# Performance work log

Measured on AMD Instinct MI355X. Metric: run time of the kernel, lower is better.

The kernel has to match this reference:

```python
import jax, jax.numpy as jnp
import numpy as np

B = 64            # graphs
N0 = 1024         # nodes per graph at level 0
DEG = 16          # avg degree
D = 128
NS = [1024, 820, 656, 525, 420, 336]  # ceil(0.8*n) cascade


def gcn(x, src, dst, valid, W, b, num_nodes):
    # x: [N,D]; src/dst: [E] int; valid: [E] float mask; W: [D,D]; b: [D]
    x = x @ W.T + b
    deg = jax.ops.segment_sum(valid, src, num_segments=num_nodes) + 1.0  # +1 self loop
    dis = jax.lax.rsqrt(deg)
    norm = dis[src] * dis[dst] * valid
    agg = jax.ops.segment_sum(norm[:, None] * x[src], dst, num_segments=num_nodes)
    return agg + (dis * dis)[:, None] * x  # self-loop term


def topk_pool(x, src, dst, valid, w, n, k):
    # PyG TopKPooling: score = tanh((x.w)/||w||); keep top ceil(ratio*n) per graph
    s = jnp.tanh((x @ w) / jnp.linalg.norm(w))
    _, idx = jax.lax.top_k(s.reshape(B, n), k)                    # [B,k] local ids
    perm = (idx + (jnp.arange(B) * n)[:, None]).reshape(-1)       # global ids
    xn = x[perm] * s[perm][:, None]
    new_id = jnp.full((B * n,), -1, jnp.int32).at[perm].set(jnp.arange(B * k, dtype=jnp.int32))
    ns_, nd_ = new_id[src], new_id[dst]
    v = valid * ((ns_ >= 0) & (nd_ >= 0)).astype(jnp.float32)
    return xn, jnp.maximum(ns_, 0), jnp.maximum(nd_, 0), v


def setup_inputs() -> dict:
    key = jax.random.key(0)
    ks = jax.random.split(key, 32)
    x = jax.random.normal(ks[0], (B * N0, D), jnp.float32)
    eg = N0 * DEG  # edges per graph
    local = jax.random.randint(ks[1], (2, B, eg), 0, N0, jnp.int32)
    edge_index = (local + (jnp.arange(B, dtype=jnp.int32) * N0)[None, :, None]).reshape(2, -1)
    batch = jnp.repeat(jnp.arange(B, dtype=jnp.int32), N0)
    sc = 1.0 / np.sqrt(D)
    inp = {"x": x, "edge_index": edge_index, "batch": batch}
    for i in range(1, 6):
        inp[f"c{i}w"] = jax.random.normal(ks[2 * i], (D, D), jnp.float32) * sc
        inp[f"c{i}b"] = jnp.zeros((D,), jnp.float32)
        inp[f"p{i}w"] = jax.random.normal(ks[2 * i + 1], (D,), jnp.float32) * sc
    inp["l1w"] = jax.random.normal(ks[20], (128, 256), jnp.float32) / np.sqrt(256)
    inp["l1b"] = jnp.zeros((128,), jnp.float32)
    inp["l2w"] = jax.random.normal(ks[21], (64, 128), jnp.float32) * sc
    inp["l2b"] = jnp.zeros((64,), jnp.float32)
    inp["l3w"] = jax.random.normal(ks[22], (2, 64), jnp.float32) / np.sqrt(64)
    inp["l3b"] = jnp.zeros((2,), jnp.float32)
    return inp


def reference(x, edge_index, batch,
              c1w, c1b, p1w, c2w, c2b, p2w, c3w, c3b, p3w,
              c4w, c4b, p4w, c5w, c5b, p5w,
              l1w, l1b, l2w, l2b, l3w, l3b):
    src, dst = edge_index[0], edge_index[1]
    valid = jnp.ones(src.shape, jnp.float32)
    layers = [(c1w, c1b, p1w), (c2w, c2b, p2w), (c3w, c3b, p3w),
              (c4w, c4b, p4w), (c5w, c5b, p5w)]
    reads = []
    for i, (cw, cb, pw) in enumerate(layers):
        n, k = NS[i], NS[i + 1]
        x = jax.nn.relu(gcn(x, src, dst, valid, cw, cb, B * n))
        x, src, dst, valid = topk_pool(x, src, dst, valid, pw, n, k)
        xk = x.reshape(B, k, D)
        reads.append(jnp.concatenate([xk.max(axis=1), xk.mean(axis=1)], axis=1))
    h = reads[0] + reads[1] + reads[2] + reads[3] + reads[4]   # [B,256]
    h = jax.nn.relu(h @ l1w.T + l1b)
    # dropout is identity in eval mode
    h = jax.nn.relu(h @ l2w.T + l2b)
    return jax.nn.log_softmax(h @ l3w.T + l3b, axis=-1)       # [B,2]
```

## Files before the change

### kernel.cpp

```cpp
#include <hip/hip_runtime.h>
#include <hip/hip_fp16.h>
#include <math.h>

#define NB 64
#define DIM 128
#define ETOT 1048576
#define EPG 16384
#define EPT 16
#define WRS 192
#define XRS 96

static const int NS_H[6] = {1024, 820, 656, 525, 420, 336};

__global__ __launch_bounds__(1024) void init_kernel(const int* __restrict__ ei,
                                  int* __restrict__ src, int* __restrict__ dst,
                                  int2* __restrict__ epack, int* __restrict__ eoff,
                                  int* __restrict__ cnt, float* __restrict__ dinv,
                                  float* __restrict__ invn, const float* __restrict__ pw0,
                                  float* __restrict__ hsum) {
    __shared__ int hs[1024], hc[1024], cur[1024];
    __shared__ float dv[1024];
    __shared__ float shf[128];
    __shared__ int wsum[16];
    int g = blockIdx.x, t = threadIdx.x;
    int lane = t & 63, wv = t >> 6;
    hs[t] = 0; hc[t] = 0;
    if (t < 256) hsum[g * 256 + t] = 0.f;
    __syncthreads();
    int b0 = g * EPG;
    int sr[EPT], dr[EPT];
#pragma unroll
    for (int q = 0; q < EPT; q++) {
        int e = b0 + q * 1024 + t;
        int s = ei[e], d = ei[ETOT + e];
        sr[q] = s; dr[q] = d;
        src[e] = s; dst[e] = d;
        atomicAdd(&hs[s & 1023], 1);
        atomicAdd(&hc[d & 1023], 1);
    }
    __syncthreads();
    int v = hc[t];
    dv[t] = rsqrtf((float)hs[t] + 1.0f);
    int s = v;
#pragma unroll
    for (int off = 1; off < 64; off <<= 1) {
        int u = __shfl_up(s, off, 64);
        if (lane >= off) s += u;
    }
    if (lane == 63) wsum[wv] = s;
    __syncthreads();
    if (wv == 0) {
        int ws = (lane < 16) ? wsum[lane] : 0;
#pragma unroll
        for (int off = 1; off < 16; off <<= 1) {
            int u = __shfl_up(ws, off, 64);
            if (lane >= off) ws += u;
        }
        if (lane < 16) wsum[lane] = ws;
    }
    __syncthreads();
    int excl = b0 + s + ((wv > 0) ? wsum[wv - 1] : 0) - v;
    eoff[g * 1024 + t] = excl;
    cnt[g * 1024 + t] = v;
    dinv[g * 1024 + t] = dv[t];
    cur[t] = excl;
    __syncthreads();
#pragma unroll
    for (int q = 0; q < EPT; q++) {
        int sl = sr[q] & 1023, dl = dr[q] & 1023;
        int pos = atomicAdd(&cur[dl], 1);
        epack[pos] = make_int2(sr[q], __float_as_int(dv[sl] * dv[dl]));
    }
    if (g == 0) {
        if (t < 128) shf[t] = pw0[t] * pw0[t];
        __syncthreads();
        for (int q = 64; q > 0; q >>= 1) {
            if (t < q) shf[t] += shf[t + q];
            __syncthreads();
        }
        if (t == 0) invn[0] = rsqrtf(shf[0]);
    }
}

__global__ __launch_bounds__(256) void linear_kernel(const float* __restrict__ x,
                              const __half* __restrict__ xh,
                              const float* __restrict__ W, const float* __restrict__ b,
                              __half* __restrict__ xH, int half_in) {
    __shared__ float Wt[32 * WRS];
    __shared__ float xT[32 * XRS];
    int tid = threadIdx.x;
    int base = blockIdx.x * 64;
    int nf = tid & 15;
    int u  = tid >> 4;
    float acc[4][8];
    {
        float bv[8];
#pragma unroll
        for (int f = 0; f < 8; f++) bv[f] = b[u * 8 + f];
#pragma unroll
        for (int i = 0; i < 4; i++)
#pragma unroll
            for (int f = 0; f < 8; f++) acc[i][f] = bv[f];
    }
    for (int kb = 0; kb < 4; kb++) {
        __syncthreads();
#pragma unroll
        for (int q = 0; q < 4; q++) {
            int i = q * 256 + tid;
            int dq = i >> 7;
            int r = i & 127;
            int s = (r >> 3) * 12 + (r & 7);
            float4 wv = *(const float4*)(W + r * 128 + kb * 32 + dq * 4);
            Wt[(dq * 4 + 0) * WRS + s] = wv.x;
            Wt[(dq * 4 + 1) * WRS + s] = wv.y;
            Wt[(dq * 4 + 2) * WRS + s] = wv.z;
            Wt[(dq * 4 + 3) * WRS + s] = wv.w;
        }
        if (half_in) {
            int dq2 = tid >> 6;
            int r = tid & 63;
            int s = (r >> 3) * 12 + (r & 7);
            uint4 hv = *(const uint4*)(xh + (size_t)(base + r) * DIM + kb * 32 + dq2 * 8);
            float2 c0 = __half22float2(*(const __half2*)&hv.x);
            float2 c1 = __half22float2(*(const __half2*)&hv.y);
            float2 c2 = __half22float2(*(const __half2*)&hv.z);
            float2 c3 = __half22float2(*(const __half2*)&hv.w);
            int cb2 = dq2 * 8;
            xT[(cb2 + 0) * XRS + s] = c0.x; xT[(cb2 + 1) * XRS + s] = c0.y;
            xT[(cb2 + 2) * XRS + s] = c1.x; xT[(cb2 + 3) * XRS + s] = c1.y;
            xT[(cb2 + 4) * XRS + s] = c2.x; xT[(cb2 + 5) * XRS + s] = c2.y;
            xT[(cb2 + 6) * XRS + s] = c3.x; xT[(cb2 + 7) * XRS + s] = c3.y;
        } else {
#pragma unroll
            for (int q = 0; q < 2; q++) {
                int i = q * 256 + tid;
                int dq = i >> 6;
                int r = i & 63;
                int s = (r >> 3) * 12 + (r & 7);
                float4 xv = *(const float4*)(x + (size_t)(base + r) * DIM + kb * 32 + dq * 4);
                xT[(dq * 4 + 0) * XRS + s] = xv.x;
                xT[(dq * 4 + 1) * XRS + s] = xv.y;
                xT[(dq * 4 + 2) * XRS + s] = xv.z;
                xT[(dq * 4 + 3) * XRS + s] = xv.w;
            }
        }
        __syncthreads();
#pragma unroll 4
        for (int d = 0; d < 32; d++) {
            float4 xv = *(const float4*)&xT[d * XRS + (nf >> 1) * 12 + (nf & 1) * 4];
            float4 wa = *(const float4*)&Wt[d * WRS + u * 12];
            float4 wb = *(const float4*)&Wt[d * WRS + u * 12 + 4];
            float xs[4] = {xv.x, xv.y, xv.z, xv.w};
            float ws[8] = {wa.x, wa.y, wa.z, wa.w, wb.x, wb.y, wb.z, wb.w};
#pragma unroll
            for (int i = 0; i < 4; i++)
#pragma unroll
                for (int f = 0; f < 8; f++)
                    acc[i][f] += xs[i] * ws[f];
        }
    }
#pragma unroll
    for (int i = 0; i < 4; i++) {
        int nd = base + nf * 4 + i;
        alignas(16) __half2 hb[4];
        hb[0] = __floats2half2_rn(acc[i][0], acc[i][1]);
        hb[1] = __floats2half2_rn(acc[i][2], acc[i][3]);
        hb[2] = __floats2half2_rn(acc[i][4], acc[i][5]);
        hb[3] = __floats2half2_rn(acc[i][6], acc[i][7]);
        *(float4*)(xH + (size_t)nd * DIM + u * 8) = *(const float4*)hb;
    }
}

__global__ void fused_agg_kernel(const __half* __restrict__ xH, const int2* __restrict__ epack,
                                 const int* __restrict__ eoff, const int* __restrict__ cnt,
                                 const float* __restrict__ dinv,
                                 const float* __restrict__ pw, const float* __restrict__ invn,
                                 float* __restrict__ xA, float* __restrict__ score, int n) {
    int t = threadIdx.x;
    int g = blockIdx.x % NB;
    int chunk = blockIdx.x / NB;
    int ln = chunk * 8 + (t >> 5);
    if (ln >= n) return;
    int node = g * n + ln;
    int lane = t & 31;
    float dsn = dinv[node];
    uint2 qs = ((const uint2*)(xH + (size_t)node * DIM))[lane];
    float2 sl = __half22float2(*(const __half2*)&qs.x);
    float2 sh = __half22float2(*(const __half2*)&qs.y);
    float w0 = dsn * dsn;
    float4 a0 = make_float4(sl.x * w0, sl.y * w0, sh.x * w0, sh.y * w0);
    float4 a1 = make_float4(0.f, 0.f, 0.f, 0.f);
    float4 a2 = make_float4(0.f, 0.f, 0.f, 0.f);
    float4 a3 = make_float4(0.f, 0.f, 0.f, 0.f);
    int s0 = eoff[node], s1 = s0 + cnt[node];
    int j = s0;
    int2 e0, e1, e2, e3;
    if (j + 3 < s1) { e0 = epack[j]; e1 = epack[j + 1]; e2 = epack[j + 2]; e3 = epack[j + 3]; }
    for (; j + 7 < s1; j += 4) {
        int2 f0 = epack[j + 4], f1 = epack[j + 5], f2 = epack[j + 6], f3 = epack[j + 7];
        uint2 x0 = ((const uint2*)(xH + (size_t)e0.x * DIM))[lane];
        uint2 x1 = ((const uint2*)(xH + (size_t)e1.x * DIM))[lane];
        uint2 x2 = ((const uint2*)(xH + (size_t)e2.x * DIM))[lane];
        uint2 x3 = ((const uint2*)(xH + (size_t)e3.x * DIM))[lane];
        float n0 = __int_as_float(e0.y), n1 = __int_as_float(e1.y);
        float n2 = __int_as_float(e2.y), n3 = __int_as_float(e3.y);
        float2 l0 = __half22float2(*(const __half2*)&x0.x), h0 = __half22float2(*(const __half2*)&x0.y);
        float2 l1 = __half22float2(*(const __half2*)&x1.x), h1 = __half22float2(*(const __half2*)&x1.y);
        float2 l2 = __half22float2(*(const __half2*)&x2.x), h2 = __half22float2(*(const __half2*)&x2.y);
        float2 l3 = __half22float2(*(const __half2*)&x3.x), h3 = __half22float2(*(const __half2*)&x3.y);
        a0.x += n0 * l0.x; a0.y += n0 * l0.y; a0.z += n0 * h0.x; a0.w += n0 * h0.y;
        a1.x += n1 * l1.x; a1.y += n1 * l1.y; a1.z += n1 * h1.x; a1.w += n1 * h1.y;
        a2.x += n2 * l2.x; a2.y += n2 * l2.y; a2.z += n2 * h2.x; a2.w += n2 * h2.y;
        a3.x += n3 * l3.x; a3.y += n3 * l3.y; a3.z += n3 * h3.x; a3.w += n3 * h3.y;
        e0 = f0; e1 = f1; e2 = f2; e3 = f3;
    }
    if (j + 3 < s1) {
        uint2 x0 = ((const uint2*)(xH + (size_t)e0.x * DIM))[lane];
        uint2 x1 = ((const uint2*)(xH + (size_t)e1.x * DIM))[lane];
        uint2 x2 = ((const uint2*)(xH + (size_t)e2.x * DIM))[lane];
        uint2 x3 = ((const uint2*)(xH + (size_t)e3.x * DIM))[lane];
        float n0 = __int_as_float(e0.y), n1 = __int_as_float(e1.y);
        float n2 = __int_as_float(e2.y), n3 = __int_as_float(e3.y);
        float2 l0 = __half22float2(*(const __half2*)&x0.x), h0 = __half22float2(*(const __half2*)&x0.y);
        float2 l1 = __half22float2(*(const __half2*)&x1.x), h1 = __half22float2(*(const __half2*)&x1.y);
        float2 l2 = __half22float2(*(const __half2*)&x2.x), h2 = __half22float2(*(const __half2*)&x2.y);
        float2 l3 = __half22float2(*(const __half2*)&x3.x), h3 = __half22float2(*(const __half2*)&x3.y);
        a0.x += n0 * l0.x; a0.y += n0 * l0.y; a0.z += n0 * h0.x; a0.w += n0 * h0.y;
        a1.x += n1 * l1.x; a1.y += n1 * l1.y; a1.z += n1 * h1.x; a1.w += n1 * h1.y;
        a2.x += n2 * l2.x; a2.y += n2 * l2.y; a2.z += n2 * h2.x; a2.w += n2 * h2.y;
        a3.x += n3 * l3.x; a3.y += n3 * l3.y; a3.z += n3 * h3.x; a3.w += n3 * h3.y;
        j += 4;
    }
    for (; j < s1; j++) {
        int2 eq = epack[j];
        float nq = __int_as_float(eq.y);
        uint2 xq = ((const uint2*)(xH + (size_t)eq.x * DIM))[lane];
        float2 lq = __half22float2(*(const __half2*)&xq.x), hq = __half22float2(*(const __half2*)&xq.y);
        a0.x += nq * lq.x; a0.y += nq * lq.y; a0.z += nq * hq.x; a0.w += nq * hq.y;
    }
    float4 acc = make_float4(fmaxf(a0.x + a1.x + a2.x + a3.x, 0.f),
                             fmaxf(a0.y + a1.y + a2.y + a3.y, 0.f),
                             fmaxf(a0.z + a1.z + a2.z + a3.z, 0.f),
                             fmaxf(a0.w + a1.w + a2.w + a3.w, 0.f));
    ((float4*)(xA + (size_t)node * DIM))[lane] = acc;
    float4 pv = ((const float4*)pw)[lane];
    float dot = acc.x * pv.x + acc.y * pv.y + acc.z * pv.z + acc.w * pv.w;
    for (int off = 16; off >= 1; off >>= 1) dot += __shfl_xor(dot, off, 32);
    if (lane == 0) score[node] = tanhf(dot * invn[0]);
}

__global__ __launch_bounds__(1024) void pool_kernel(const float* __restrict__ score,
                              const float* __restrict__ xA, __half* __restrict__ xn,
                              float* __restrict__ h, int* __restrict__ src,
                              int* __restrict__ dst, int2* __restrict__ epack,
                              int* __restrict__ eoff, int* __restrict__ cnt,
                              float* __restrict__ dinv, const float* __restrict__ pwN,
                              float* __restrict__ invn, int n, int k, int last,
                              const float* __restrict__ l1w, const float* __restrict__ l1b,
                              const float* __restrict__ l2w, const float* __restrict__ l2b,
                              const float* __restrict__ l3w, const float* __restrict__ l3b,
                              float* __restrict__ out) {
    __shared__ float keyS[2][1024];
    __shared__ int idxS[2][1024];
    __shared__ int nid[1024];
    __shared__ float4 smax[32][33];
    __shared__ float4 ssum[32][33];
    __shared__ int hs[1024], hc[1024], cur[1024];
    __shared__ float dv[1024];
    __shared__ float shf[128];
    __shared__ int wsum[16];
    __shared__ float hr[256], h1[128], h2[64], lz[2];
    int g = blockIdx.x, t = threadIdx.x;
    int lane = t & 63, wv = t >> 6;
    int b0 = g * EPG, gn = g * n, gk = g * k;
    float k_r = (t < n) ? score[g * n + t] : -2.0f;
    int i_r = t;
    hs[t] = 0; hc[t] = 0;
    int se[EPT], de[EPT];
    if (!last) {
#pragma unroll
        for (int q = 0; q < EPT; q++) {
            int e = b0 + q * 1024 + t;
            se[q] = src[e];
            de[q] = dst[e];
        }
    }
    int par = 0;
    for (unsigned ksz = 2; ksz <= 1024; ksz <<= 1) {
        for (unsigned jj = ksz >> 1; jj > 0; jj >>= 1) {
            float kq; int iq;
            if (jj >= 64) {
                keyS[par][t] = k_r; idxS[par][t] = i_r;
                __syncthreads();
                kq = keyS[par][t ^ jj]; iq = idxS[par][t ^ jj];
                par ^= 1;
            } else {
                kq = __shfl_xor(k_r, (int)jj, 64);
                iq = __shfl_xor(i_r, (int)jj, 64);
            }
            bool mineFirst = (k_r > kq) || (k_r == kq && i_r < iq);
            bool up = ((t & ksz) == 0);
            bool iAmLower = ((t & jj) == 0);
            bool keepMine = (iAmLower == up) ? mineFirst : !mineFirst;
            if (!keepMine) { k_r = kq; i_r = iq; }
        }
    }
    keyS[0][t] = k_r; idxS[0][t] = i_r;
    nid[i_r] = (t < (unsigned)k) ? t : -1;
    __syncthreads();
    int lane4 = t & 31;
    int ch = t >> 5;
    float4 mx = make_float4(-INFINITY, -INFINITY, -INFINITY, -INFINITY);
    float4 sm = make_float4(0.f, 0.f, 0.f, 0.f);
    for (int j = ch; j < k; j += 32) {
        int row = idxS[0][j];
        float sval = keyS[0][j];
        float4 vv = ((const float4*)(xA + ((size_t)g * n + row) * DIM))[lane4];
        vv.x *= sval; vv.y *= sval; vv.z *= sval; vv.w *= sval;
        if (!last) {
            __half2 p0 = __floats2half2_rn(vv.x, vv.y);
            __half2 p1 = __floats2half2_rn(vv.z, vv.w);
            uint2 pk;
            pk.x = *(unsigned int*)&p0;
            pk.y = *(unsigned int*)&p1;
            ((uint2*)(xn + ((size_t)g * k + j) * DIM))[lane4] = pk;
        }
        mx.x = fmaxf(mx.x, vv.x); mx.y = fmaxf(mx.y, vv.y);
        mx.z = fmaxf(mx.z, vv.z); mx.w = fmaxf(mx.w, vv.w);
        sm.x += vv.x; sm.y += vv.y; sm.z += vv.z; sm.w += vv.w;
    }
    smax[ch][lane4] = mx;
    ssum[ch][lane4] = sm;
    __syncthreads();
    for (int s = 16; s >= 1; s >>= 1) {
        if (ch < s) {
            float4 a = smax[ch][lane4], bb = smax[ch + s][lane4];
            a.x = fmaxf(a.x, bb.x); a.y = fmaxf(a.y, bb.y);
            a.z = fmaxf(a.z, bb.z); a.w = fmaxf(a.w, bb.w);
            smax[ch][lane4] = a;
            float4 c = ssum[ch][lane4], d = ssum[ch + s][lane4];
            c.x += d.x; c.y += d.y; c.z += d.z; c.w += d.w;
            ssum[ch][lane4] = c;
        }
        __syncthreads();
    }
    if (ch == 0) {
        float4 m = smax[0][lane4];
        float4 s4 = ssum[0][lane4];
        float invk = 1.0f / (float)k;
        int f0 = lane4 * 4;
        if (!last) {
            float* hp = h + g * 256;
            hp[f0 + 0] += m.x; hp[f0 + 1] += m.y; hp[f0 + 2] += m.z; hp[f0 + 3] += m.w;
            hp[128 + f0 + 0] += s4.x * invk; hp[128 + f0 + 1] += s4.y * invk;
            hp[128 + f0 + 2] += s4.z * invk; hp[128 + f0 + 3] += s4.w * invk;
        } else {
            const float* hp = h + g * 256;
            hr[f0 + 0] = hp[f0 + 0] + m.x; hr[f0 + 1] = hp[f0 + 1] + m.y;
            hr[f0 + 2] = hp[f0 + 2] + m.z; hr[f0 + 3] = hp[f0 + 3] + m.w;
            hr[128 + f0 + 0] = hp[128 + f0 + 0] + s4.x * invk;
            hr[128 + f0 + 1] = hp[128 + f0 + 1] + s4.y * invk;
            hr[128 + f0 + 2] = hp[128 + f0 + 2] + s4.z * invk;
            hr[128 + f0 + 3] = hp[128 + f0 + 3] + s4.w * invk;
        }
    }
    if (last) {
        __syncthreads();
        if (t < 128) {
            float a1 = l1b[t];
            for (int d = 0; d < 256; d++) a1 += hr[d] * l1w[t * 256 + d];
            h1[t] = fmaxf(a1, 0.f);
        }
        __syncthreads();
        if (t < 64) {
            float a2 = l2b[t];
            for (int d = 0; d < 128; d++) a2 += h1[d] * l2w[t * 128 + d];
            h2[t] = fmaxf(a2, 0.f);
        }
        __syncthreads();
        if (t < 2) {
            float a3 = l3b[t];
            for (int d = 0; d < 64; d++) a3 += h2[d] * l3w[t * 64 + d];
            lz[t] = a3;
        }
        __syncthreads();
        if (t < 2) {
            float z0 = lz[0], z1 = lz[1];
            float m = fmaxf(z0, z1);
            float lse = m + logf(expf(z0 - m) + expf(z1 - m));
            out[g * 2 + t] = lz[t] - lse;
        }
        return;
    }
    int sr[EPT], dr[EPT];
#pragma unroll
    for (int q = 0; q < EPT; q++) {
        int e = b0 + q * 1024 + t;
        int s = se[q];
        int s2 = -1, d2 = -1;
        if (s >= 0) {
            s2 = nid[s - gn];
            d2 = nid[de[q] - gn];
            if (s2 >= 0 && d2 >= 0) {
                src[e] = gk + s2;
                dst[e] = gk + d2;
                atomicAdd(&hs[s2], 1);
                atomicAdd(&hc[d2], 1);
            } else {
                src[e] = -1;
                dst[e] = -1;
                s2 = -1;
            }
        }
        sr[q] = s2; dr[q] = d2;
    }
    __syncthreads();
    int v = (t < k) ? hc[t] : 0;
    if (t < k) dv[t] = rsqrtf((float)hs[t] + 1.0f);
    int s = v;
#pragma unroll
    for (int off = 1; off < 64; off <<= 1) {
        int u = __shfl_up(s, off, 64);
        if (lane >= off) s += u;
    }
    if (lane == 63) wsum[wv] = s;
    __syncthreads();
    if (wv == 0) {
        int ws = (lane < 16) ? wsum[lane] : 0;
#pragma unroll
        for (int off = 1; off < 16; off <<= 1) {
            int u = __shfl_up(ws, off, 64);
            if (lane >= off) ws += u;
        }
        if (lane < 16) wsum[lane] = ws;
    }
    __syncthreads();
    if (t < k) {
        int excl = b0 + s + ((wv > 0) ? wsum[wv - 1] : 0) - v;
        eoff[gk + t] = excl;
        cnt[gk + t] = v;
        dinv[gk + t] = dv[t];
        cur[t] = excl;
    }
    __syncthreads();
#pragma unroll
    for (int q = 0; q < EPT; q++) {
        if (sr[q] >= 0) {
            int pos = atomicAdd(&cur[dr[q]], 1);
            epack[pos] = make_int2(gk + sr[q], __float_as_int(dv[sr[q]] * dv[dr[q]]));
        }
    }
    if (g == 0) {
        if (t < 128) shf[t] = pwN[t] * pwN[t];
        __syncthreads();
        for (int q = 64; q > 0; q >>= 1) {
            if (t < q) shf[t] += shf[t + q];
            __syncthreads();
        }
        if (t == 0) invn[0] = rsqrtf(shf[0]);
    }
}

extern "C" void kernel_launch(void* const* d_in, const int* in_sizes, int n_in,
                              void* d_out, int out_size, void* d_ws, size_t ws_size,
                              hipStream_t stream) {
    const float* x_in = (const float*)d_in[0];
    const int* edge_index = (const int*)d_in[1];
    const float *cw[5], *cb[5], *pw[5];
    for (int i = 0; i < 5; i++) {
        cw[i] = (const float*)d_in[3 + 3 * i];
        cb[i] = (const float*)d_in[4 + 3 * i];
        pw[i] = (const float*)d_in[5 + 3 * i];
    }
    const float* l1w = (const float*)d_in[18];
    const float* l1b = (const float*)d_in[19];
    const float* l2w = (const float*)d_in[20];
    const float* l2b = (const float*)d_in[21];
    const float* l3w = (const float*)d_in[22];
    const float* l3b = (const float*)d_in[23];
    float* out = (float*)d_out;

    char* w = (char*)d_ws;
    float*  xA    = (float*)w;  w += (size_t)65536 * DIM * 4;
    __half* xB    = (__half*)w; w += (size_t)65536 * DIM * 4;
    __half* xH    = (__half*)w; w += (size_t)65536 * DIM * 4;
    int*   src   = (int*)w;   w += (size_t)ETOT * 4;
    int*   dst   = (int*)w;   w += (size_t)ETOT * 4;
    int2*  epack = (int2*)w;  w += (size_t)ETOT * 8;
    int*   cnt   = (int*)w;   w += (size_t)65536 * 4;
    int*   eoff  = (int*)w;   w += (size_t)65536 * 4;
    float* dinv  = (float*)w; w += (size_t)65536 * 4;
    float* score = (float*)w; w += (size_t)65536 * 4;
    float* hsum  = (float*)w; w += (size_t)NB * 256 * 4;
    float* invn  = (float*)w; w += 4;

    init_kernel<<<NB, 1024, 0, stream>>>(edge_index, src, dst, epack, eoff, cnt, dinv,
                                         invn, pw[0], hsum);

    for (int i = 0; i < 5; i++) {
        int n = NS_H[i], k = NS_H[i + 1];
        int N = NB * n;

        linear_kernel<<<N / 64, 256, 0, stream>>>(x_in, xB, cw[i], cb[i], xH, (i > 0) ? 1 : 0);
        int gpb = (n + 7) / 8;
        fused_agg_kernel<<<NB * gpb, 256, 0, stream>>>(xH, epack, eoff, cnt, dinv, pw[i],
                                                       invn, xA, score, n);
        pool_kernel<<<NB, 1024, 0, stream>>>(score, xA, xB, hsum, src, dst, epack, eoff,
                                             cnt, dinv, (i < 4) ? pw[i + 1] : pw[i], invn,
                                             n, k, (i == 4) ? 1 : 0,
                                             l1w, l1b, l2w, l2b, l3w, l3b, out);
    }
}
```

Measured before the change: 522.3 us.

## Split pooled gather/readout into wide gather kernel with atomic readout and head kernel

```diff
diff --git a/kernel.cpp b/kernel.cpp
--- a/kernel.cpp
+++ b/kernel.cpp
@@ -12,12 +12,21 @@
 
 static const int NS_H[6] = {1024, 820, 656, 525, 420, 336};
 
+__device__ __forceinline__ unsigned fxform(float f) {
+    int b = __float_as_int(f);
+    return (b >= 0) ? ((unsigned)b | 0x80000000u) : ~(unsigned)b;
+}
+__device__ __forceinline__ float fxinv(unsigned u) {
+    int b = (u & 0x80000000u) ? (int)(u ^ 0x80000000u) : (int)~u;
+    return __int_as_float(b);
+}
+
 __global__ __launch_bounds__(1024) void init_kernel(const int* __restrict__ ei,
                                   int* __restrict__ src, int* __restrict__ dst,
                                   int2* __restrict__ epack, int* __restrict__ eoff,
                                   int* __restrict__ cnt, float* __restrict__ dinv,
                                   float* __restrict__ invn, const float* __restrict__ pw0,
-                                  float* __restrict__ hsum) {
+                                  unsigned* __restrict__ maxb, float* __restrict__ sumb) {
     __shared__ int hs[1024], hc[1024], cur[1024];
     __shared__ float dv[1024];
     __shared__ float shf[128];
@@ -25,7 +34,8 @@
     int g = blockIdx.x, t = threadIdx.x;
     int lane = t & 63, wv = t >> 6;
     hs[t] = 0; hc[t] = 0;
-    if (t < 256) hsum[g * 256 + t] = 0.f;
+    int idx = g * 1024 + t;
+    if (idx < 5 * NB * 128) { maxb[idx] = 0x007FFFFFu; sumb[idx] = 0.f; }
     __syncthreads();
     int b0 = g * EPG;
     int sr[EPT], dr[EPT];
@@ -175,7 +185,7 @@
                                  const int* __restrict__ eoff, const int* __restrict__ cnt,
                                  const float* __restrict__ dinv,
                                  const float* __restrict__ pw, const float* __restrict__ invn,
-                                 float* __restrict__ xA, float* __restrict__ score, int n) {
+                                 __half* __restrict__ xA, float* __restrict__ score, int n) {
     int t = threadIdx.x;
     int g = blockIdx.x % NB;
     int chunk = blockIdx.x / NB;
@@ -242,7 +252,12 @@
                              fmaxf(a0.y + a1.y + a2.y + a3.y, 0.f),
                              fmaxf(a0.z + a1.z + a2.z + a3.z, 0.f),
                              fmaxf(a0.w + a1.w + a2.w + a3.w, 0.f));
-    ((float4*)(xA + (size_t)node * DIM))[lane] = acc;
+    __half2 o0 = __floats2half2_rn(acc.x, acc.y);
+    __half2 o1 = __floats2half2_rn(acc.z, acc.w);
+    uint2 pk;
+    pk.x = *(unsigned int*)&o0;
+    pk.y = *(unsigned int*)&o1;
+    ((uint2*)(xA + (size_t)node * DIM))[lane] = pk;
     float4 pv = ((const float4*)pw)[lane];
     float dot = acc.x * pv.x + acc.y * pv.y + acc.z * pv.z + acc.w * pv.w;
     for (int off = 16; off >= 1; off >>= 1) dot += __shfl_xor(dot, off, 32);
@@ -250,26 +265,19 @@
 }
 
 __global__ __launch_bounds__(1024) void pool_kernel(const float* __restrict__ score,
-                              const float* __restrict__ xA, __half* __restrict__ xn,
-                              float* __restrict__ h, int* __restrict__ src,
-                              int* __restrict__ dst, int2* __restrict__ epack,
-                              int* __restrict__ eoff, int* __restrict__ cnt,
-                              float* __restrict__ dinv, const float* __restrict__ pwN,
-                              float* __restrict__ invn, int n, int k, int last,
-                              const float* __restrict__ l1w, const float* __restrict__ l1b,
-                              const float* __restrict__ l2w, const float* __restrict__ l2b,
-                              const float* __restrict__ l3w, const float* __restrict__ l3b,
-                              float* __restrict__ out) {
+                              int* __restrict__ permG, float* __restrict__ svalG,
+                              int* __restrict__ src, int* __restrict__ dst,
+                              int2* __restrict__ epack, int* __restrict__ eoff,
+                              int* __restrict__ cnt, float* __restrict__ dinv,
+                              const float* __restrict__ pwN, float* __restrict__ invn,
+                              int n, int k, int last) {
     __shared__ float keyS[2][1024];
     __shared__ int idxS[2][1024];
     __shared__ int nid[1024];
-    __shared__ float4 smax[32][33];
-    __shared__ float4 ssum[32][33];
     __shared__ int hs[1024], hc[1024], cur[1024];
     __shared__ float dv[1024];
     __shared__ float shf[128];
     __shared__ int wsum[16];
-    __shared__ float hr[256], h1[128], h2[64], lz[2];
     int g = blockIdx.x, t = threadIdx.x;
     int lane = t & 63, wv = t >> 6;
     int b0 = g * EPG, gn = g * n, gk = g * k;
@@ -305,93 +313,10 @@
             if (!keepMine) { k_r = kq; i_r = iq; }
         }
     }
-    keyS[0][t] = k_r; idxS[0][t] = i_r;
     nid[i_r] = (t < (unsigned)k) ? t : -1;
-    __syncthreads();
-    int lane4 = t & 31;
-    int ch = t >> 5;
-    float4 mx = make_float4(-INFINITY, -INFINITY, -INFINITY, -INFINITY);
-    float4 sm = make_float4(0.f, 0.f, 0.f, 0.f);
-    for (int j = ch; j < k; j += 32) {
-        int row = idxS[0][j];
-        float sval = keyS[0][j];
-        float4 vv = ((const float4*)(xA + ((size_t)g * n + row) * DIM))[lane4];
-        vv.x *= sval; vv.y *= sval; vv.z *= sval; vv.w *= sval;
-        if (!last) {
-            __half2 p0 = __floats2half2_rn(vv.x, vv.y);
-            __half2 p1 = __floats2half2_rn(vv.z, vv.w);
-            uint2 pk;
-            pk.x = *(unsigned int*)&p0;
-            pk.y = *(unsigned int*)&p1;
-            ((uint2*)(xn + ((size_t)g * k + j) * DIM))[lane4] = pk;
-        }
-        mx.x = fmaxf(mx.x, vv.x); mx.y = fmaxf(mx.y, vv.y);
-        mx.z = fmaxf(mx.z, vv.z); mx.w = fmaxf(mx.w, vv.w);
-        sm.x += vv.x; sm.y += vv.y; sm.z += vv.z; sm.w += vv.w;
-    }
-    smax[ch][lane4] = mx;
-    ssum[ch][lane4] = sm;
-    __syncthreads();
-    for (int s = 16; s >= 1; s >>= 1) {
-        if (ch < s) {
-            float4 a = smax[ch][lane4], bb = smax[ch + s][lane4];
-            a.x = fmaxf(a.x, bb.x); a.y = fmaxf(a.y, bb.y);
-            a.z = fmaxf(a.z, bb.z); a.w = fmaxf(a.w, bb.w);
-            smax[ch][lane4] = a;
-            float4 c = ssum[ch][lane4], d = ssum[ch + s][lane4];
-            c.x += d.x; c.y += d.y; c.z += d.z; c.w += d.w;
-            ssum[ch][lane4] = c;
-        }
-        __syncthreads();
-    }
-    if (ch == 0) {
-        float4 m = smax[0][lane4];
-        float4 s4 = ssum[0][lane4];
-        float invk = 1.0f / (float)k;
-        int f0 = lane4 * 4;
-        if (!last) {
-            float* hp = h + g * 256;
-            hp[f0 + 0] += m.x; hp[f0 + 1] += m.y; hp[f0 + 2] += m.z; hp[f0 + 3] += m.w;
-            hp[128 + f0 + 0] += s4.x * invk; hp[128 + f0 + 1] += s4.y * invk;
-            hp[128 + f0 + 2] += s4.z * invk; hp[128 + f0 + 3] += s4.w * invk;
-        } else {
-            const float* hp = h + g * 256;
-            hr[f0 + 0] = hp[f0 + 0] + m.x; hr[f0 + 1] = hp[f0 + 1] + m.y;
-            hr[f0 + 2] = hp[f0 + 2] + m.z; hr[f0 + 3] = hp[f0 + 3] + m.w;
-            hr[128 + f0 + 0] = hp[128 + f0 + 0] + s4.x * invk;
-            hr[128 + f0 + 1] = hp[128 + f0 + 1] + s4.y * invk;
-            hr[128 + f0 + 2] = hp[128 + f0 + 2] + s4.z * invk;
-            hr[128 + f0 + 3] = hp[128 + f0 + 3] + s4.w * invk;
-        }
-    }
-    if (last) {
-        __syncthreads();
-        if (t < 128) {
-            float a1 = l1b[t];
-            for (int d = 0; d < 256; d++) a1 += hr[d] * l1w[t * 256 + d];
-            h1[t] = fmaxf(a1, 0.f);
-        }
-        __syncthreads();
-        if (t < 64) {
-            float a2 = l2b[t];
-            for (int d = 0; d < 128; d++) a2 += h1[d] * l2w[t * 128 + d];
-            h2[t] = fmaxf(a2, 0.f);
-        }
-        __syncthreads();
-        if (t < 2) {
-            float a3 = l3b[t];
-            for (int d = 0; d < 64; d++) a3 += h2[d] * l3w[t * 64 + d];
-            lz[t] = a3;
-        }
-        __syncthreads();
-        if (t < 2) {
-            float z0 = lz[0], z1 = lz[1];
-            float m = fmaxf(z0, z1);
-            float lse = m + logf(expf(z0 - m) + expf(z1 - m));
-            out[g * 2 + t] = lz[t] - lse;
-        }
-        return;
-    }
+    if (t < k) { permG[gk + t] = i_r; svalG[gk + t] = k_r; }
+    __syncthreads();
+    if (last) return;
     int sr[EPT], dr[EPT];
 #pragma unroll
     for (int q = 0; q < EPT; q++) {
@@ -461,6 +386,110 @@
     }
 }
 
+__global__ __launch_bounds__(256) void gather_kernel(const __half* __restrict__ xA,
+                                const int* __restrict__ permG, const float* __restrict__ svalG,
+                                __half* __restrict__ xn,
+                                unsigned* __restrict__ maxbL, float* __restrict__ sumbL,
+                                int n, int k, int last) {
+    __shared__ float4 smx[8][33];
+    __shared__ float4 ssm[8][33];
+    int t = threadIdx.x;
+    int g = blockIdx.x % NB;
+    int chunk = blockIdx.x / NB;
+    int j = chunk * 8 + (t >> 5);
+    int lane = t & 31;
+    int ch = t >> 5;
+    float4 mx = make_float4(-INFINITY, -INFINITY, -INFINITY, -INFINITY);
+    float4 sm = make_float4(0.f, 0.f, 0.f, 0.f);
+    if (j < k) {
+        int row = permG[g * k + j];
+        float s = svalG[g * k + j];
+        uint2 hv = ((const uint2*)(xA + ((size_t)g * n + row) * DIM))[lane];
+        float2 lo = __half22float2(*(const __half2*)&hv.x);
+        float2 hi = __half22float2(*(const __half2*)&hv.y);
+        float4 vv = make_float4(lo.x * s, lo.y * s, hi.x * s, hi.y * s);
+        if (!last) {
+            __half2 p0 = __floats2half2_rn(vv.x, vv.y);
+            __half2 p1 = __floats2half2_rn(vv.z, vv.w);
+            uint2 pk;
+            pk.x = *(unsigned int*)&p0;
+            pk.y = *(unsigned int*)&p1;
+            ((uint2*)(xn + ((size_t)g * k + j) * DIM))[lane] = pk;
+        }
+        mx = vv; sm = vv;
+    }
+    smx[ch][lane] = mx;
+    ssm[ch][lane] = sm;
+    __syncthreads();
+    for (int s = 4; s >= 1; s >>= 1) {
+        if (ch < s) {
+            float4 a = smx[ch][lane], bb = smx[ch + s][lane];
+            a.x = fmaxf(a.x, bb.x); a.y = fmaxf(a.y, bb.y);
+            a.z = fmaxf(a.z, bb.z); a.w = fmaxf(a.w, bb.w);
+            smx[ch][lane] = a;
+            float4 c = ssm[ch][lane], d = ssm[ch + s][lane];
+            c.x += d.x; c.y += d.y; c.z += d.z; c.w += d.w;
+            ssm[ch][lane] = c;
+        }
+        __syncthreads();
+    }
+    if (ch == 0) {
+        float4 m = smx[0][lane];
+        float4 s4 = ssm[0][lane];
+        int f0 = g * 128 + lane * 4;
+        atomicMax(&maxbL[f0 + 0], fxform(m.x));
+        atomicMax(&maxbL[f0 + 1], fxform(m.y));
+        atomicMax(&maxbL[f0 + 2], fxform(m.z));
+        atomicMax(&maxbL[f0 + 3], fxform(m.w));
+        atomicAdd(&sumbL[f0 + 0], s4.x);
+        atomicAdd(&sumbL[f0 + 1], s4.y);
+        atomicAdd(&sumbL[f0 + 2], s4.z);
+        atomicAdd(&sumbL[f0 + 3], s4.w);
+    }
+}
+
+__global__ __launch_bounds__(128) void head_kernel(const unsigned* __restrict__ maxb,
+                              const float* __restrict__ sumb,
+                              const float* __restrict__ l1w, const float* __restrict__ l1b,
+                              const float* __restrict__ l2w, const float* __restrict__ l2b,
+                              const float* __restrict__ l3w, const float* __restrict__ l3b,
+                              float* __restrict__ out) {
+    __shared__ float hr[256], h1[128], h2[64], lz[2];
+    int g = blockIdx.x, t = threadIdx.x;
+    const float invk[5] = {1.f / 820.f, 1.f / 656.f, 1.f / 525.f, 1.f / 420.f, 1.f / 336.f};
+    float mxs = 0.f, sms = 0.f;
+#pragma unroll
+    for (int L = 0; L < 5; L++) {
+        mxs += fxinv(maxb[(L * NB + g) * 128 + t]);
+        sms += sumb[(L * NB + g) * 128 + t] * invk[L];
+    }
+    hr[t] = mxs;
+    hr[128 + t] = sms;
+    __syncthreads();
+    float a1 = l1b[t];
+    for (int d = 0; d < 256; d++) a1 += hr[d] * l1w[t * 256 + d];
+    h1[t] = fmaxf(a1, 0.f);
+    __syncthreads();
+    if (t < 64) {
+        float a2 = l2b[t];
+        for (int d = 0; d < 128; d++) a2 += h1[d] * l2w[t * 128 + d];
+        h2[t] = fmaxf(a2, 0.f);
+    }
+    __syncthreads();
+    if (t < 2) {
+        float a3 = l3b[t];
+        for (int d = 0; d < 64; d++) a3 += h2[d] * l3w[t * 64 + d];
+        lz[t] = a3;
+    }
+    __syncthreads();
+    if (t < 2) {
+        float z0 = lz[0], z1 = lz[1];
+        float m = fmaxf(z0, z1);
+        float lse = m + logf(expf(z0 - m) + expf(z1 - m));
+        out[g * 2 + t] = lz[t] - lse;
+    }
+}
+
 extern "C" void kernel_launch(void* const* d_in, const int* in_sizes, int n_in,
                               void* d_out, int out_size, void* d_ws, size_t ws_size,
                               hipStream_t stream) {
@@ -481,9 +510,9 @@
     float* out = (float*)d_out;
 
     char* w = (char*)d_ws;
-    float*  xA    = (float*)w;  w += (size_t)65536 * DIM * 4;
-    __half* xB    = (__half*)w; w += (size_t)65536 * DIM * 4;
-    __half* xH    = (__half*)w; w += (size_t)65536 * DIM * 4;
+    __half* xA    = (__half*)w; w += (size_t)65536 * DIM * 2;
+    __half* xB    = (__half*)w; w += (size_t)65536 * DIM * 2;
+    __half* xH    = (__half*)w; w += (size_t)65536 * DIM * 2;
     int*   src   = (int*)w;   w += (size_t)ETOT * 4;
     int*   dst   = (int*)w;   w += (size_t)ETOT * 4;
     int2*  epack = (int2*)w;  w += (size_t)ETOT * 8;
@@ -491,23 +520,32 @@
     int*   eoff  = (int*)w;   w += (size_t)65536 * 4;
     float* dinv  = (float*)w; w += (size_t)65536 * 4;
     float* score = (float*)w; w += (size_t)65536 * 4;
-    float* hsum  = (float*)w; w += (size_t)NB * 256 * 4;
+    int*   perm  = (int*)w;   w += (size_t)65536 * 4;
+    float* sval  = (float*)w; w += (size_t)65536 * 4;
+    unsigned* maxb = (unsigned*)w; w += (size_t)5 * NB * 128 * 4;
+    float* sumb  = (float*)w; w += (size_t)5 * NB * 128 * 4;
     float* invn  = (float*)w; w += 4;
 
     init_kernel<<<NB, 1024, 0, stream>>>(edge_index, src, dst, epack, eoff, cnt, dinv,
-                                         invn, pw[0], hsum);
+                                         invn, pw[0], maxb, sumb);
 
     for (int i = 0; i < 5; i++) {
         int n = NS_H[i], k = NS_H[i + 1];
         int N = NB * n;
+        int last = (i == 4) ? 1 : 0;
 
         linear_kernel<<<N / 64, 256, 0, stream>>>(x_in, xB, cw[i], cb[i], xH, (i > 0) ? 1 : 0);
         int gpb = (n + 7) / 8;
         fused_agg_kernel<<<NB * gpb, 256, 0, stream>>>(xH, epack, eoff, cnt, dinv, pw[i],
                                                        invn, xA, score, n);
-        pool_kernel<<<NB, 1024, 0, stream>>>(score, xA, xB, hsum, src, dst, epack, eoff,
+        pool_kernel<<<NB, 1024, 0, stream>>>(score, perm, sval, src, dst, epack, eoff,
                                              cnt, dinv, (i < 4) ? pw[i + 1] : pw[i], invn,
-                                             n, k, (i == 4) ? 1 : 0,
-                                             l1w, l1b, l2w, l2b, l3w, l3b, out);
-    }
-}
+                                             n, k, last);
+        int gpk = (k + 7) / 8;
+        gather_kernel<<<NB * gpk, 256, 0, stream>>>(xA, perm, sval, xB,
+                                                    maxb + (size_t)i * NB * 128,
+                                                    sumb + (size_t)i * NB * 128,
+                                                    n, k, last);
+    }
+    head_kernel<<<NB, 128, 0, stream>>>(maxb, sumb, l1w, l1b, l2w, l2b, l3w, l3b, out);
+}
```

Result: slower. 558.4 us (+6.9%).
